# Optimization experiments

Measured on AMD Instinct MI355X. Metric: run time of the kernel, lower is better.

## Reference

```python
import jax, jax.numpy as jnp
import numpy as np

B, C, H, W = 4, 512, 64, 208
HID = 512          # params.text_hidden_dim; must equal C for view(1,C,H,-1)
DS = 16            # 1/scale_factor for nearest downsample of the mask
N_REG = 4          # four region-indexed attention modules


def setup_inputs() -> dict:
    key = jax.random.key(0)
    ks = jax.random.split(key, 7)
    image_feature = jax.random.normal(ks[0], (B, C, H, W), dtype=jnp.float32)
    text_feat = jax.random.normal(ks[1], (N_REG, B, HID), dtype=jnp.float32)
    # Mask is constant per (full-res) column so that each region's pixel count
    # is divisible by H, as the original view(1, C, H, -1) requires.
    col_labels = jax.random.randint(ks[2], (B, W * DS), 1, N_REG + 1)
    text_mask = jnp.broadcast_to(
        col_labels[:, None, None, :], (B, 1, H * DS, W * DS)
    ).astype(jnp.int32)
    # Per-region MHA params (nn.Linear weights, no bias assumed).
    Wq = jax.random.normal(ks[3], (N_REG, C, HID), dtype=jnp.float32) * (C ** -0.5)
    Wk = jax.random.normal(ks[4], (N_REG, HID, HID), dtype=jnp.float32) * (HID ** -0.5)
    Wv = jax.random.normal(ks[5], (N_REG, HID, HID), dtype=jnp.float32) * (HID ** -0.5)
    Wo = jax.random.normal(ks[6], (N_REG, HID, C), dtype=jnp.float32) * (HID ** -0.5)
    return {
        "image_feature": image_feature,
        "text_feat": text_feat,
        "text_mask": text_mask,
        "Wq": Wq,
        "Wk": Wk,
        "Wv": Wv,
        "Wo": Wo,
    }


def reference(image_feature, text_feat, text_mask, Wq, Wk, Wv, Wo):
    # F.interpolate(scale=1/16, mode='nearest') == strided slicing for integer stride.
    mask_ds = text_mask[:, 0, ::DS, ::DS]          # [B, H, W]
    col_labels = mask_ds[:, 0, :]                  # [B, W] (mask is column-constant)
    # Cross-attention of every region pixel (query) against ONE text token z
    # (single key/value): softmax over a length-1 axis is identically 1, so
    # attn_out = Wo @ (Wv @ z) for every pixel, and Wq/Wk receive zero gradient.
    # With the residual connection: out_pixel = x_pixel + (z Wv) Wo per region.
    delta = jnp.einsum('rbh,rhd,rdc->brc', text_feat, Wv, Wo)          # [B, R, C]
    d_col = jnp.take_along_axis(delta, (col_labels - 1)[:, :, None], axis=1)  # [B, W, C]
    out = image_feature + d_col.transpose(0, 2, 1)[:, :, None, :]      # [B, C, H, W]
    # The torch code concatenates regions along width in sorted-unique label
    # order, i.e. columns are permuted by (label, original column) -- a stable
    # argsort of the column labels.
    order = jnp.argsort(col_labels, axis=1, stable=True)               # [B, W]
    return jnp.take_along_axis(out, order[:, None, None, :], axis=3)
```

## Files before the change

### kernel.cpp

```cpp
#include <hip/hip_runtime.h>

#define B_ 4
#define C_ 512
#define H_ 64
#define W_ 208
#define HID_ 512
#define NREG_ 4
#define DS_ 16


__global__ __launch_bounds__(256) void prep1_kernel(
    const float* __restrict__ tf, const float* __restrict__ Wv,
    const int* __restrict__ mask, float* __restrict__ tmp, int* __restrict__ swl) {
  int blk = blockIdx.x, tid = threadIdx.x;
  if (blk < 32) {
    int r = blk >> 3, h0 = (blk & 7) * 64;
    __shared__ float tf_s[B_][64];
    {
      int b = tid >> 6, hh = tid & 63;
      tf_s[b][hh] = tf[(r * B_ + b) * HID_ + h0 + hh];
    }
    __syncthreads();
    float acc[B_][2] = {};
    for (int hh = 0; hh < 64; ++hh) {
      const float* row = Wv + (size_t)(r * HID_ + h0 + hh) * HID_;
      float w1 = row[tid], w2 = row[tid + 256];
#pragma unroll
      for (int b = 0; b < B_; ++b) {
        float t = tf_s[b][hh];
        acc[b][0] += t * w1;
        acc[b][1] += t * w2;
      }
    }
#pragma unroll
    for (int b = 0; b < B_; ++b) {
      atomicAdd(&tmp[(b * NREG_ + r) * HID_ + tid], acc[b][0]);
      atomicAdd(&tmp[(b * NREG_ + r) * HID_ + tid + 256], acc[b][1]);
    }
  } else {
    int b = blk - 32;
    const size_t mb = (size_t)b * (H_ * DS_) * (W_ * DS_);
    int w = tid;
    int l = (w < W_) ? (mask[mb + (size_t)w * DS_] - 1) : -1;
    int wave = tid >> 6, lane = tid & 63;
    unsigned long long bal[NREG_];
    __shared__ int wcnt[4][NREG_];
#pragma unroll
    for (int r = 0; r < NREG_; ++r) bal[r] = __ballot(l == r);
    if (lane < NREG_) wcnt[wave][lane] = __popcll(bal[lane]);
    __syncthreads();
    if (w < W_) {
      int pos = 0;
#pragma unroll
      for (int q = 0; q < NREG_; ++q) {
        int tot = wcnt[0][q] + wcnt[1][q] + wcnt[2][q] + wcnt[3][q];
        if (q < l) pos += tot;
      }
#pragma unroll
      for (int v = 0; v < 4; ++v)
        if (v < wave) pos += wcnt[v][l];
      pos += __popcll(bal[l] & ((1ull << lane) - 1ull));
      swl[b * W_ + pos] = w | (l << 16);
    }
  }
}

__global__ __launch_bounds__(256) void prep2_kernel(
    const float* __restrict__ tmp, const float* __restrict__ Wo,
    float* __restrict__ delta) {
  int blk = blockIdx.x, tid = threadIdx.x;
  int r = blk >> 3, d0 = (blk & 7) * 64;
  __shared__ float tmp_s[B_][64];
  {
    int b = tid >> 6, dd = tid & 63;
    tmp_s[b][dd] = tmp[(b * NREG_ + r) * HID_ + d0 + dd];
  }
  __syncthreads();
  float acc[B_][2] = {};
  for (int dd = 0; dd < 64; ++dd) {
    const float* row = Wo + (size_t)(r * HID_ + d0 + dd) * C_;
    float w1 = row[tid], w2 = row[tid + 256];
#pragma unroll
    for (int b = 0; b < B_; ++b) {
      float t = tmp_s[b][dd];
      acc[b][0] += t * w1;
      acc[b][1] += t * w2;
    }
  }
#pragma unroll
  for (int b = 0; b < B_; ++b) {
    atomicAdd(&delta[(b * NREG_ + b ? b * NREG_ * 0 : 0) + (b * NREG_ + r) * C_ - (b * NREG_ + r) * C_ + (b * NREG_ + r) * C_ + tid], acc[b][0]);
    atomicAdd(&delta[(b * NREG_ + r) * C_ + tid + 256], acc[b][1]);
  }
}

#define ROWS_ 32
#define RCH_ (W_ / 4)
#define CHUNKS_ (ROWS_ * RCH_)
__global__ __launch_bounds__(256) void apply_kernel(
    const float* __restrict__ img, const float* __restrict__ delta,
    const int* __restrict__ swl, float* __restrict__ out) {
  int r0 = blockIdx.x * ROWS_;
  int b = r0 >> 15;
  int c = (r0 >> 6) & (C_ - 1);
  int tid = threadIdx.x;
  __shared__ float tile[ROWS_ * W_];
  __shared__ int swl_s[W_];
  __shared__ float dsel_s[NREG_];
  const float4* src = (const float4*)(img + (size_t)r0 * W_);
  float4* tile4 = (float4*)tile;
  for (int i = tid; i < CHUNKS_; i += 256) tile4[i] = src[i];
  if (tid < W_) swl_s[tid] = swl[b * W_ + tid];
  if (tid < NREG_) dsel_s[tid] = delta[(b * NREG_ + tid) * C_ + c];
  __syncthreads();
  float d0 = dsel_s[0], d1 = dsel_s[1], d2 = dsel_s[2], d3 = dsel_s[3];
  float4* dst = (float4*)(out + (size_t)r0 * W_);
  for (int i = tid; i < CHUNKS_; i += 256) {
    int row_local = i / RCH_;
    int j = i - row_local * RCH_;
    int base = row_local * W_;
    float res[4];
#pragma unroll
    for (int k = 0; k < 4; ++k) {
      int pl = swl_s[j * 4 + k];
      int s = pl & 0xFFFF;
      int r = pl >> 16;
      float dv = (r == 0) ? d0 : (r == 1) ? d1 : (r == 2) ? d2 : d3;
      res[k] = tile[base + s] + dv;
    }
    dst[i] = make_float4(res[0], res[1], res[2], res[3]);
  }
}

extern "C" void kernel_launch(void* const* d_in, const int* in_sizes, int n_in,
                              void* d_out, int out_size, void* d_ws, size_t ws_size,
                              hipStream_t stream) {
  const float* img  = (const float*)d_in[0];
  const float* tf   = (const float*)d_in[1];
  const int*   mask = (const int*)d_in[2];
  const float* Wv   = (const float*)d_in[5];
  const float* Wo   = (const float*)d_in[6];
  float* delta = (float*)d_ws;
  float* tmp   = (float*)((char*)d_ws + 32768);
  int*   swl   = (int*)((char*)d_ws + 65536);
  float* out   = (float*)d_out;

  hipMemsetAsync(d_ws, 0, 65536, stream);
  prep1_kernel<<<36, 256, 0, stream>>>(tf, Wv, mask, tmp, swl);
  prep2_kernel<<<32, 256, 0, stream>>>(tmp, Wo, delta);
  apply_kernel<<<(B_ * C_ * H_) / ROWS_, 256, 0, stream>>>(img, delta, swl, out);
}
```

Measured before the change: 256.0 us.

## Split prep GEMVs across 256 blocks with in-block reduction; halve apply rows

```diff
diff --git a/kernel.cpp b/kernel.cpp
--- a/kernel.cpp
+++ b/kernel.cpp
@@ -9,36 +9,34 @@
 #define DS_ 16
 
 
-__global__ __launch_bounds__(256) void prep1_kernel(
+__global__ __launch_bounds__(256) void prepA_kernel(
     const float* __restrict__ tf, const float* __restrict__ Wv,
     const int* __restrict__ mask, float* __restrict__ tmp, int* __restrict__ swl) {
   int blk = blockIdx.x, tid = threadIdx.x;
-  if (blk < 32) {
-    int r = blk >> 3, h0 = (blk & 7) * 64;
+  if (blk < 256) {
+    int r = blk >> 6;
+    int h0 = ((blk >> 3) & 7) * 64;
+    int d0 = (blk & 7) * 64;
+    int g = tid >> 6, dd = tid & 63;
     __shared__ float tf_s[B_][64];
-    {
-      int b = tid >> 6, hh = tid & 63;
-      tf_s[b][hh] = tf[(r * B_ + b) * HID_ + h0 + hh];
-    }
+    __shared__ float red[4][B_][64];
+    tf_s[g][dd] = tf[(r * B_ + g) * HID_ + h0 + dd];
     __syncthreads();
-    float acc[B_][2] = {};
-    for (int hh = 0; hh < 64; ++hh) {
-      const float* row = Wv + (size_t)(r * HID_ + h0 + hh) * HID_;
-      float w1 = row[tid], w2 = row[tid + 256];
+    float acc[B_] = {};
+    for (int hh = g * 16; hh < g * 16 + 16; ++hh) {
+      float w = Wv[(size_t)(r * HID_ + h0 + hh) * HID_ + d0 + dd];
 #pragma unroll
-      for (int b = 0; b < B_; ++b) {
-        float t = tf_s[b][hh];
-        acc[b][0] += t * w1;
-        acc[b][1] += t * w2;
-      }
+      for (int b = 0; b < B_; ++b) acc[b] += tf_s[b][hh] * w;
     }
 #pragma unroll
-    for (int b = 0; b < B_; ++b) {
-      atomicAdd(&tmp[(b * NREG_ + r) * HID_ + tid], acc[b][0]);
-      atomicAdd(&tmp[(b * NREG_ + r) * HID_ + tid + 256], acc[b][1]);
+    for (int b = 0; b < B_; ++b) red[g][b][dd] = acc[b];
+    __syncthreads();
+    {
+      float s = red[0][g][dd] + red[1][g][dd] + red[2][g][dd] + red[3][g][dd];
+      atomicAdd(&tmp[(g * NREG_ + r) * HID_ + d0 + dd], s);
     }
   } else {
-    int b = blk - 32;
+    int b = blk - 256;
     const size_t mb = (size_t)b * (H_ * DS_) * (W_ * DS_);
     int w = tid;
     int l = (w < W_) ? (mask[mb + (size_t)w * DS_] - 1) : -1;
@@ -65,36 +63,34 @@
   }
 }
 
-__global__ __launch_bounds__(256) void prep2_kernel(
+__global__ __launch_bounds__(256) void prepB_kernel(
     const float* __restrict__ tmp, const float* __restrict__ Wo,
     float* __restrict__ delta) {
   int blk = blockIdx.x, tid = threadIdx.x;
-  int r = blk >> 3, d0 = (blk & 7) * 64;
+  int r = blk >> 6;
+  int d0 = ((blk >> 3) & 7) * 64;
+  int c0 = (blk & 7) * 64;
+  int g = tid >> 6, cc = tid & 63;
   __shared__ float tmp_s[B_][64];
-  {
-    int b = tid >> 6, dd = tid & 63;
-    tmp_s[b][dd] = tmp[(b * NREG_ + r) * HID_ + d0 + dd];
-  }
+  __shared__ float red[4][B_][64];
+  tmp_s[g][cc] = tmp[(g * NREG_ + r) * HID_ + d0 + cc];
   __syncthreads();
-  float acc[B_][2] = {};
-  for (int dd = 0; dd < 64; ++dd) {
-    const float* row = Wo + (size_t)(r * HID_ + d0 + dd) * C_;
-    float w1 = row[tid], w2 = row[tid + 256];
+  float acc[B_] = {};
+  for (int dd = g * 16; dd < g * 16 + 16; ++dd) {
+    float w = Wo[(size_t)(r * HID_ + d0 + dd) * C_ + c0 + cc];
 #pragma unroll
-    for (int b = 0; b < B_; ++b) {
-      float t = tmp_s[b][dd];
-      acc[b][0] += t * w1;
-      acc[b][1] += t * w2;
-    }
+    for (int b = 0; b < B_; ++b) acc[b] += tmp_s[b][dd] * w;
   }
 #pragma unroll
-  for (int b = 0; b < B_; ++b) {
-    atomicAdd(&delta[(b * NREG_ + b ? b * NREG_ * 0 : 0) + (b * NREG_ + r) * C_ - (b * NREG_ + r) * C_ + (b * NREG_ + r) * C_ + tid], acc[b][0]);
-    atomicAdd(&delta[(b * NREG_ + r) * C_ + tid + 256], acc[b][1]);
+  for (int b = 0; b < B_; ++b) red[g][b][cc] = acc[b];
+  __syncthreads();
+  {
+    float s = red[0][g][cc] + red[1][g][cc] + red[2][g][cc] + red[3][g][cc];
+    atomicAdd(&delta[(g * NREG_ + r) * C_ + c0 + cc], s);
   }
 }
 
-#define ROWS_ 32
+#define ROWS_ 16
 #define RCH_ (W_ / 4)
 #define CHUNKS_ (ROWS_ * RCH_)
 __global__ __launch_bounds__(256) void apply_kernel(
@@ -146,7 +142,7 @@
   float* out   = (float*)d_out;
 
   hipMemsetAsync(d_ws, 0, 65536, stream);
-  prep1_kernel<<<36, 256, 0, stream>>>(tf, Wv, mask, tmp, swl);
-  prep2_kernel<<<32, 256, 0, stream>>>(tmp, Wo, delta);
+  prepA_kernel<<<260, 256, 0, stream>>>(tf, Wv, mask, tmp, swl);
+  prepB_kernel<<<256, 256, 0, stream>>>(tmp, Wo, delta);
   apply_kernel<<<(B_ * C_ * H_) / ROWS_, 256, 0, stream>>>(img, delta, swl, out);
 }
```

New measurement: 242.1 us. 1.06x faster.
